# Kernel tuning notes

Measured on AMD Instinct MI355X. Metric: run time of the kernel, lower is better.

Reference implementation:

```python
import jax, jax.numpy as jnp
import numpy as np

B = 32768
ARITY = 6
E = 256          # embedding_size
NF = 512         # num_filters
NR = 50000       # num_roles
NV = 50000       # num_values
BN_EPS = 1e-5


def setup_inputs() -> dict:
    key = jax.random.key(0)
    ks = jax.random.split(key, 7)
    bound = (1.0 / E) ** 0.5
    # padding_idx=0 rows zeroed, matching torch Embedding(padding_idx=0)
    emb_roles = jax.random.uniform(ks[0], (NR, E), minval=-bound, maxval=bound).at[0].set(0.0)
    emb_values = jax.random.uniform(ks[1], (NV, E), minval=-bound, maxval=bound).at[2].set(0.0).at[0].set(0.0)
    # truncated_normal(std=0.1) approximated by clipped normal
    conv1_w = jnp.clip(jax.random.normal(ks[2], (NF, 2, E)), -2.0, 2.0) * 0.1
    conv2_w = jnp.clip(jax.random.normal(ks[3], (NF, 5, E)), -2.0, 2.0) * 0.1
    fc_w = jax.random.normal(ks[4], (1, NF)) * (2.0 / (NF + 1)) ** 0.5  # xavier_normal
    x_batch = jax.random.randint(ks[5], (B, 2 * ARITY), 0, NR, dtype=jnp.int32)
    return dict(
        x_batch=x_batch,
        arity=ARITY,
        emb_roles=emb_roles,
        emb_values=emb_values,
        conv1_w=conv1_w,
        conv1_b=jnp.zeros((NF,), jnp.float32),
        bn1_gamma=jnp.ones((NF,), jnp.float32),
        bn1_beta=jnp.zeros((NF,), jnp.float32),
        conv2_w=conv2_w,
        conv2_b=jnp.zeros((NF,), jnp.float32),
        bn2_gamma=jnp.ones((NF,), jnp.float32),
        bn2_beta=jnp.zeros((NF,), jnp.float32),
        fc_w=fc_w,
        fc_b=jnp.zeros((1,), jnp.float32),
    )


def _bn_relu(x, gamma, beta):
    # x: [B, K, F]; BatchNorm2d in training mode: per-(window-call, channel) stats over batch
    m = jnp.mean(x, axis=0, keepdims=True)
    v = jnp.var(x, axis=0, keepdims=True)  # biased, matches torch normalization
    return jax.nn.relu(gamma * (x - m) * jax.lax.rsqrt(v + BN_EPS) + beta)


def _forward(x_batch, arity, emb_roles, emb_values,
             conv1_w, conv1_b, bn1_gamma, bn1_beta,
             conv2_w, conv2_b, bn2_gamma, bn2_beta, fc_w, fc_b):
    roles = x_batch[:, 0::2]   # [B, arity]
    values = x_batch[:, 1::2]  # [B, arity]
    fr = emb_roles[roles[:, :2]]    # [B, 2, E]
    fv = emb_values[values[:, :2]]  # [B, 2, E]

    # conv1 on two (value, role) windows; kernel (2, E) collapses to a contraction over (2, E)
    win1 = jnp.stack([
        jnp.stack([fv[:, 0], fr[:, 0]], axis=1),
        jnp.stack([fv[:, 1], fr[:, 0]], axis=1),
    ], axis=1)  # [B, 2, 2, E]
    out1 = jnp.einsum('bkre,fre->bkf', win1, conv1_w) + conv1_b
    out1 = _bn_relu(out1, bn1_gamma, bn1_beta)  # [B, 2, F]

    if arity > 2:
        K = arity - 2
        kr = emb_roles[roles[:, 2:]]    # [B, K, E]
        kv = emb_values[values[:, 2:]]  # [B, K, E]
        hrt = jnp.stack([fv[:, 0], fr[:, 0], fv[:, 1]], axis=1)  # [B, 3, E]
        win2 = jnp.concatenate([
            jnp.broadcast_to(hrt[:, None], (hrt.shape[0], K, 3, hrt.shape[-1])),
            kr[:, :, None],
            kv[:, :, None],
        ], axis=2)  # [B, K, 5, E]
        out2 = jnp.einsum('bkre,fre->bkf', win2, conv2_w) + conv2_b
        out2 = _bn_relu(out2, bn2_gamma, bn2_beta)  # [B, K, F]
        allw = jnp.concatenate([out1, out2], axis=1)  # [B, 2+K, F]
    else:
        allw = out1

    min_val = jnp.min(allw, axis=1)  # [B, F]
    return min_val @ fc_w.T + fc_b   # [B, 1]


def reference(x_batch, arity, emb_roles, emb_values,
              conv1_w, conv1_b, bn1_gamma, bn1_beta,
              conv2_w, conv2_b, bn2_gamma, bn2_beta, fc_w, fc_b):
    return _forward(x_batch, arity, emb_roles, emb_values,
                    conv1_w, conv1_b, bn1_gamma, bn1_beta,
                    conv2_w, conv2_b, bn2_gamma, bn2_beta, fc_w, fc_b)
```

## Files before the change

### kernel.cpp

```cpp
#include <hip/hip_runtime.h>
#include <hip/hip_bf16.h>


typedef __hip_bfloat16 bf16;
typedef short bf16x8 __attribute__((ext_vector_type(8)));
typedef float f32x4 __attribute__((ext_vector_type(4)));

#define BATCH 32768

__device__ __forceinline__ unsigned short f2b(float f) {
    union { float f; unsigned u; } v; v.f = f;
    unsigned r = v.u + 0x7fffu + ((v.u >> 16) & 1u);
    return (unsigned short)(r >> 16);
}

__device__ __forceinline__ float b2f(unsigned short u) {
    union { unsigned x; float f; } v; v.x = ((unsigned)u) << 16;
    return v.f;
}

__global__ __launch_bounds__(256)
void cvt_kernel(const float* __restrict__ src, unsigned short* __restrict__ dst, int n4)
{
    int i = blockIdx.x * 256 + threadIdx.x;
    if (i >= n4) return;
    float4 v = ((const float4*)src)[i];
    ushort4 h;
    h.x = f2b(v.x); h.y = f2b(v.y); h.z = f2b(v.z); h.w = f2b(v.w);
    ((ushort4*)dst)[i] = h;
}

template<bool FINAL>
__global__ __launch_bounds__(512, 2)
void pass_kernel(const int* __restrict__ x, const bf16* __restrict__ embR,
                 const bf16* __restrict__ embV, const bf16* __restrict__ W1b,
                 const bf16* __restrict__ W2b, float* __restrict__ accum,
                 const float* __restrict__ coef, const float* __restrict__ fcw,
                 float* __restrict__ outacc)
{
    __shared__ __align__(16) short Ash[128 * 72];
    __shared__ __align__(16) short Bsh[256 * 72];
    __shared__ int xsh[384];
    __shared__ __align__(16) float scr[4096];

    const int tid = threadIdx.x;
    const int lin = blockIdx.x;
    const int mt  = (lin >> 4) * 8 + (lin & 7);
    const int nb  = ((lin >> 3) & 1) * 256;
    const int b0  = mt * 32;

    for (int i = tid; i < 384; i += 512) xsh[i] = x[b0 * 12 + i];
    if constexpr (!FINAL)
        for (int i = tid; i < 3072; i += 512) scr[i] = 0.f;
    __syncthreads();

    const int lane = tid & 63;
    const int wv   = tid >> 6;
    const int wmb  = (wv >> 2) * 64;
    const int wnb  = (wv & 3) * 64;
    const int quad = lane >> 4;
    const int l16  = lane & 15;

    auto stageA = [&](int seg, int col, bool g1) {
        #pragma unroll
        for (int it = 0; it < 2; ++it) {
            int flat = tid + it * 512;
            int row  = flat >> 3;
            int off8 = flat & 7;
            int idx; const bf16* tab;
            if (g1) {
                int vr = row & 63, bl = vr >> 1, kk = vr & 1;
                if (seg == 0) { idx = xsh[bl * 12 + 2 * kk + 1]; tab = embV; }
                else          { idx = xsh[bl * 12];              tab = embR; }
            } else {
                int bl = row >> 2, kk = row & 3;
                switch (seg) {
                    case 0:  idx = xsh[bl * 12 + 1];          tab = embV; break;
                    case 1:  idx = xsh[bl * 12 + 0];          tab = embR; break;
                    case 2:  idx = xsh[bl * 12 + 3];          tab = embV; break;
                    case 3:  idx = xsh[bl * 12 + 2 * kk + 4]; tab = embR; break;
                    default: idx = xsh[bl * 12 + 2 * kk + 5]; tab = embV; break;
                }
            }
            uint4 v = *((const uint4*)(tab + (size_t)idx * 256 + col) + off8);
            *(uint4*)&Ash[row * 72 + off8 * 8] = v;
        }
    };
    auto stageB = [&](const bf16* W, int stride, int col) {
        #pragma unroll
        for (int it = 0; it < 4; ++it) {
            int flat = tid + it * 512;
            int fr   = flat >> 3;
            int off8 = flat & 7;
            uint4 v = *((const uint4*)(W + (size_t)(nb + fr) * stride + col) + off8);
            *(uint4*)&Bsh[fr * 72 + off8 * 8] = v;
        }
    };
    auto mma = [&](f32x4 (&acc)[4][4]) {
        #pragma unroll
        for (int ks = 0; ks < 64; ks += 32) {
            bf16x8 af[4], bf_[4];
            #pragma unroll
            for (int t = 0; t < 4; ++t)
                af[t]  = *(const bf16x8*)&Ash[(wmb + t * 16 + l16) * 72 + ks + quad * 8];
            #pragma unroll
            for (int t = 0; t < 4; ++t)
                bf_[t] = *(const bf16x8*)&Bsh[(wnb + t * 16 + l16) * 72 + ks + quad * 8];
            #pragma unroll
            for (int i = 0; i < 4; ++i)
                #pragma unroll
                for (int j = 0; j < 4; ++j)
                    acc[i][j] = __builtin_amdgcn_mfma_f32_16x16x32_bf16(
                        af[i], bf_[j], acc[i][j], 0, 0, 0);
        }
    };

    f32x4 acc[4][4];

    #pragma unroll
    for (int i = 0; i < 4; ++i)
        #pragma unroll
        for (int j = 0; j < 4; ++j)
            acc[i][j] = (f32x4){0.f, 0.f, 0.f, 0.f};
    #pragma unroll 1
    for (int ch = 0; ch < 8; ++ch) {
        stageA(ch >> 2, (ch & 3) * 64, true);
        stageB(W1b, 512, ch * 64);
        __syncthreads();
        mma(acc);
        __syncthreads();
    }
    if (wv < 4) {
        if constexpr (!FINAL) {
            #pragma unroll
            for (int j = 0; j < 4; ++j) {
                int fl = wnb + j * 16 + l16;
                #pragma unroll
                for (int r = 0; r < 4; ++r) {
                    float sr = 0.f, qr = 0.f;
                    #pragma unroll
                    for (int i = 0; i < 4; ++i) {
                        float v = acc[i][j][r];
                        sr += v; qr += v * v;
                    }
                    atomicAdd(&scr[(r & 1) * 256 + fl], sr);
                    atomicAdd(&scr[1536 + (r & 1) * 256 + fl], qr);
                }
            }
        } else {
            unsigned short* m1s = (unsigned short*)scr;
            #pragma unroll
            for (int j = 0; j < 4; ++j) {
                int fl = wnb + j * 16 + l16, f = nb + fl;
                float a0 = coef[f],       c0 = coef[3072 + f];
                float a1 = coef[512 + f], c1 = coef[3584 + f];
                #pragma unroll
                for (int i = 0; i < 4; ++i)
                    #pragma unroll
                    for (int rp = 0; rp < 2; ++rp) {
                        int bl = i * 8 + quad * 2 + rp;
                        float v0 = fmaxf(a0 * acc[i][j][rp * 2]     + c0, 0.f);
                        float v1 = fmaxf(a1 * acc[i][j][rp * 2 + 1] + c1, 0.f);
                        m1s[bl * 256 + fl] = f2b(fminf(v0, v1));
                    }
            }
        }
    }

    #pragma unroll
    for (int i = 0; i < 4; ++i)
        #pragma unroll
        for (int j = 0; j < 4; ++j)
            acc[i][j] = (f32x4){0.f, 0.f, 0.f, 0.f};
    #pragma unroll 1
    for (int ch = 0; ch < 20; ++ch) {
        stageA(ch >> 2, (ch & 3) * 64, false);
        stageB(W2b, 1280, ch * 64);
        __syncthreads();
        mma(acc);
        __syncthreads();
    }
    if constexpr (!FINAL) {
        #pragma unroll
        for (int j = 0; j < 4; ++j) {
            int fl = wnb + j * 16 + l16;
            #pragma unroll
            for (int r = 0; r < 4; ++r) {
                float sr = 0.f, qr = 0.f;
                #pragma unroll
                for (int i = 0; i < 4; ++i) {
                    float v = acc[i][j][r];
                    sr += v; qr += v * v;
                }
                atomicAdd(&scr[(2 + r) * 256 + fl], sr);
                atomicAdd(&scr[1536 + (2 + r) * 256 + fl], qr);
            }
        }
        __syncthreads();
        for (int i2 = tid; i2 < 1536; i2 += 512) {
            int kw = i2 >> 8, fl = i2 & 255;
            atomicAdd(&accum[kw * 512 + nb + fl], scr[i2]);
            atomicAdd(&accum[3072 + kw * 512 + nb + fl], scr[1536 + i2]);
        }
    } else {
        const unsigned short* m1s = (const unsigned short*)scr;
        float dp[4] = {0.f, 0.f, 0.f, 0.f};
        #pragma unroll
        for (int j = 0; j < 4; ++j) {
            int fl = wnb + j * 16 + l16, f = nb + fl;
            float a[4], c[4];
            #pragma unroll
            for (int r = 0; r < 4; ++r) {
                a[r] = coef[(2 + r) * 512 + f];
                c[r] = coef[3072 + (2 + r) * 512 + f];
            }
            float fw = fcw[f];
            #pragma unroll
            for (int i = 0; i < 4; ++i) {
                int bb = (wmb >> 2) + i * 4 + quad;
                float mv = 1e30f;
                #pragma unroll
                for (int r = 0; r < 4; ++r)
                    mv = fminf(mv, fmaxf(a[r] * acc[i][j][r] + c[r], 0.f));
                mv = fminf(mv, b2f(m1s[bb * 256 + fl]));
                dp[i] += mv * fw;
            }
        }
        #pragma unroll
        for (int i = 0; i < 4; ++i) {
            float v = dp[i];
            v += __shfl_xor(v, 1); v += __shfl_xor(v, 2);
            v += __shfl_xor(v, 4); v += __shfl_xor(v, 8);
            if (l16 == 0)
                atomicAdd(&outacc[b0 + (wmb >> 2) + i * 4 + quad], v);
        }
    }
}

__global__ void bncoef_kernel(const float* __restrict__ accum,
                              const float* __restrict__ g1, const float* __restrict__ be1,
                              const float* __restrict__ g2, const float* __restrict__ be2,
                              float* __restrict__ coef)
{
    int id = blockIdx.x * 256 + threadIdx.x;
    if (id >= 3072) return;
    int kw = id >> 9, f = id & 511;
    float mean = accum[id] * (1.f / BATCH);
    float var  = accum[3072 + id] * (1.f / BATCH) - mean * mean;
    float g  = kw < 2 ? g1[f] : g2[f];
    float be = kw < 2 ? be1[f] : be2[f];
    float a  = g * rsqrtf(var + 1e-5f);
    coef[id] = a;
    coef[3072 + id] = be - a * mean;
}

__global__ void finish_kernel(const float* __restrict__ outacc,
                              const float* __restrict__ fcb, float* __restrict__ out)
{
    int b = blockIdx.x * 256 + threadIdx.x;
    if (b < BATCH)
        out[b] = outacc[b] + fcb[0];
}

extern "C" void kernel_launch(void* const* d_in, const int* in_sizes, int n_in,
                              void* d_out, int out_size, void* d_ws, size_t ws_size,
                              hipStream_t stream)
{
    (void)in_sizes; (void)n_in; (void)out_size; (void)ws_size;
    const int*   x    = (const int*)  d_in[0];
    const float* embR = (const float*)d_in[2];
    const float* embV = (const float*)d_in[3];
    const float* W1   = (const float*)d_in[4];
    const float* g1   = (const float*)d_in[6];
    const float* be1  = (const float*)d_in[7];
    const float* W2   = (const float*)d_in[8];
    const float* g2   = (const float*)d_in[10];
    const float* be2  = (const float*)d_in[11];
    const float* fcw  = (const float*)d_in[12];
    const float* fcb  = (const float*)d_in[13];

    char* wsb = (char*)d_ws;
    float* accum  = (float*)wsb;
    float* coef   = accum + 6144;
    float* outacc = coef + 6144;
    bf16*  Wbf1   = (bf16*)(wsb + 180224);
    bf16*  Wbf2   = (bf16*)(wsb + 704512);
    bf16*  embRb  = (bf16*)(wsb + 2015232);
    bf16*  embVb  = (bf16*)(wsb + 27615232);

    hipMemsetAsync(accum, 0, 6144 * sizeof(float), stream);
    hipMemsetAsync(outacc, 0, BATCH * sizeof(float), stream);
    cvt_kernel<<<256, 256, 0, stream>>>(W1, (unsigned short*)Wbf1, 65536);
    cvt_kernel<<<640, 256, 0, stream>>>(W2, (unsigned short*)Wbf2, 163840);
    cvt_kernel<<<12500, 256, 0, stream>>>(embR, (unsigned short*)embRb, 3200000);
    cvt_kernel<<<12500, 256, 0, stream>>>(embV, (unsigned short*)embVb, 3200000);

    pass_kernel<false><<<2048, 512, 0, stream>>>(
        x, embRb, embVb, Wbf1, Wbf2, accum, nullptr, nullptr, nullptr);
    bncoef_kernel<<<12, 256, 0, stream>>>(accum, g1, be1, g2, be2, coef);
    pass_kernel<true><<<2048, 512, 0, stream>>>(
        x, embRb, embVb, Wbf1, Wbf2, nullptr, coef, fcw, outacc);
    finish_kernel<<<128, 256, 0, stream>>>(outacc, fcb, (float*)d_out);
}
```

Before: 896.1 us.

## Fuse conv stages into one prefetched loop with full-filter 1024-thread blocks

Each block now covers all 512 filters with 16 waves instead of splitting filters across two blocks, so each embedding row is gathered once rather than twice. The conv1 and conv2 chunk loops merge into a single 28-stage loop. Global loads for the next stage are issued into registers before the current MFMA step, so gather latency overlaps with compute. The cost is more LDS per block (a doubled B tile and scratch), which likely allows only one block per CU, plus heavier barriers across 16 waves and extra register pressure from the prefetch buffers.

```diff
diff --git a/kernel.cpp b/kernel.cpp
--- a/kernel.cpp
+++ b/kernel.cpp
@@ -31,7 +31,7 @@
 }
 
 template<bool FINAL>
-__global__ __launch_bounds__(512, 2)
+__global__ __launch_bounds__(1024, 4)
 void pass_kernel(const int* __restrict__ x, const bf16* __restrict__ embR,
                  const bf16* __restrict__ embV, const bf16* __restrict__ W1b,
                  const bf16* __restrict__ W2b, float* __restrict__ accum,
@@ -39,64 +39,92 @@
                  float* __restrict__ outacc)
 {
     __shared__ __align__(16) short Ash[128 * 72];
-    __shared__ __align__(16) short Bsh[256 * 72];
+    __shared__ __align__(16) short Bsh[512 * 72];
     __shared__ int xsh[384];
-    __shared__ __align__(16) float scr[4096];
+    __shared__ __align__(16) float scr[8192];
 
     const int tid = threadIdx.x;
-    const int lin = blockIdx.x;
-    const int mt  = (lin >> 4) * 8 + (lin & 7);
-    const int nb  = ((lin >> 3) & 1) * 256;
-    const int b0  = mt * 32;
-
-    for (int i = tid; i < 384; i += 512) xsh[i] = x[b0 * 12 + i];
+    const int b0  = blockIdx.x * 32;
+
+    for (int i = tid; i < 384; i += 1024) xsh[i] = x[b0 * 12 + i];
     if constexpr (!FINAL)
-        for (int i = tid; i < 3072; i += 512) scr[i] = 0.f;
+        for (int i = tid; i < 6144; i += 1024) scr[i] = 0.f;
     __syncthreads();
 
     const int lane = tid & 63;
     const int wv   = tid >> 6;
-    const int wmb  = (wv >> 2) * 64;
-    const int wnb  = (wv & 3) * 64;
+    const int wmb  = (wv >> 3) * 64;
+    const int wnb  = (wv & 7) * 64;
     const int quad = lane >> 4;
     const int l16  = lane & 15;
-
-    auto stageA = [&](int seg, int col, bool g1) {
-        #pragma unroll
-        for (int it = 0; it < 2; ++it) {
-            int flat = tid + it * 512;
-            int row  = flat >> 3;
-            int off8 = flat & 7;
-            int idx; const bf16* tab;
-            if (g1) {
-                int vr = row & 63, bl = vr >> 1, kk = vr & 1;
-                if (seg == 0) { idx = xsh[bl * 12 + 2 * kk + 1]; tab = embV; }
-                else          { idx = xsh[bl * 12];              tab = embR; }
-            } else {
-                int bl = row >> 2, kk = row & 3;
-                switch (seg) {
-                    case 0:  idx = xsh[bl * 12 + 1];          tab = embV; break;
-                    case 1:  idx = xsh[bl * 12 + 0];          tab = embR; break;
-                    case 2:  idx = xsh[bl * 12 + 3];          tab = embV; break;
-                    case 3:  idx = xsh[bl * 12 + 2 * kk + 4]; tab = embR; break;
-                    default: idx = xsh[bl * 12 + 2 * kk + 5]; tab = embV; break;
-                }
-            }
-            uint4 v = *((const uint4*)(tab + (size_t)idx * 256 + col) + off8);
-            *(uint4*)&Ash[row * 72 + off8 * 8] = v;
+    const int arow = tid >> 3;
+    const int aoff = tid & 7;
+
+    auto issue = [&](int st, uint4& a, uint4 (&b)[4]) {
+        int idx; const bf16* tab;
+        if (st < 8) {
+            int seg = st >> 2;
+            int vr = arow & 63, bl = vr >> 1, kk = vr & 1;
+            if (seg == 0) { idx = xsh[bl * 12 + 2 * kk + 1]; tab = embV; }
+            else          { idx = xsh[bl * 12];              tab = embR; }
+            a = *((const uint4*)(tab + (size_t)idx * 256 + (st & 3) * 64) + aoff);
+            #pragma unroll
+            for (int it = 0; it < 4; ++it) {
+                int flat = tid + it * 1024, fr = flat >> 3, o8 = flat & 7;
+                b[it] = *((const uint4*)(W1b + (size_t)fr * 512 + st * 64) + o8);
+            }
+        } else if (st < 20) {
+            int ch = st - 8, seg = ch >> 2;
+            int bl = arow >> 2;
+            if (seg == 0)      { idx = xsh[bl * 12 + 1]; tab = embV; }
+            else if (seg == 1) { idx = xsh[bl * 12 + 0]; tab = embR; }
+            else               { idx = xsh[bl * 12 + 3]; tab = embV; }
+            a = *((const uint4*)(tab + (size_t)idx * 256 + (ch & 3) * 64) + aoff);
+            #pragma unroll
+            for (int it = 0; it < 4; ++it) {
+                int flat = tid + it * 1024, fr = flat >> 3, o8 = flat & 7;
+                b[it] = *((const uint4*)(W2b + (size_t)fr * 1280 + ch * 64) + o8);
+            }
+        } else {
+            int ch = st - 20, seg = ch >> 2;
+            int bl = arow >> 2, kk = arow & 3;
+            if (seg == 0) { idx = xsh[bl * 12 + 2 * kk + 4]; tab = embR; }
+            else          { idx = xsh[bl * 12 + 2 * kk + 5]; tab = embV; }
+            a = *((const uint4*)(tab + (size_t)idx * 256 + (ch & 3) * 64) + aoff);
+            #pragma unroll
+            for (int it = 0; it < 4; ++it) {
+                int flat = tid + it * 1024, fr = flat >> 3, o8 = flat & 7;
+                b[it] = *((const uint4*)(W2b + (size_t)fr * 1280 + 768 + ch * 64) + o8);
+            }
         }
     };
-    auto stageB = [&](const bf16* W, int stride, int col) {
+    auto wA = [&](const uint4& a) {
+        *(uint4*)&Ash[arow * 72 + aoff * 8] = a;
+    };
+    auto wB = [&](const uint4 (&b)[4]) {
         #pragma unroll
         for (int it = 0; it < 4; ++it) {
-            int flat = tid + it * 512;
-            int fr   = flat >> 3;
-            int off8 = flat & 7;
-            uint4 v = *((const uint4*)(W + (size_t)(nb + fr) * stride + col) + off8);
-            *(uint4*)&Bsh[fr * 72 + off8 * 8] = v;
+            int flat = tid + it * 1024, fr = flat >> 3, o8 = flat & 7;
+            *(uint4*)&Bsh[fr * 72 + o8 * 8] = b[it];
         }
     };
-    auto mma = [&](f32x4 (&acc)[4][4]) {
+
+    f32x4 acc[4][4];
+    #pragma unroll
+    for (int i = 0; i < 4; ++i)
+        #pragma unroll
+        for (int j = 0; j < 4; ++j)
+            acc[i][j] = (f32x4){0.f, 0.f, 0.f, 0.f};
+
+    uint4 pa, pb[4];
+    issue(0, pa, pb);
+
+    #pragma unroll 1
+    for (int st = 0; st < 28; ++st) {
+        wA(pa); wB(pb);
+        uint4 na, nb[4];
+        if (st < 27) issue(st + 1, na, nb);
+        __syncthreads();
         #pragma unroll
         for (int ks = 0; ks < 64; ks += 32) {
             bf16x8 af[4], bf_[4];
@@ -113,73 +141,57 @@
                     acc[i][j] = __builtin_amdgcn_mfma_f32_16x16x32_bf16(
                         af[i], bf_[j], acc[i][j], 0, 0, 0);
         }
-    };
-
-    f32x4 acc[4][4];
-
-    #pragma unroll
-    for (int i = 0; i < 4; ++i)
-        #pragma unroll
-        for (int j = 0; j < 4; ++j)
-            acc[i][j] = (f32x4){0.f, 0.f, 0.f, 0.f};
-    #pragma unroll 1
-    for (int ch = 0; ch < 8; ++ch) {
-        stageA(ch >> 2, (ch & 3) * 64, true);
-        stageB(W1b, 512, ch * 64);
+        if (st == 7) {
+            if (wv < 8) {
+                if constexpr (!FINAL) {
+                    #pragma unroll
+                    for (int j = 0; j < 4; ++j) {
+                        int fl = wnb + j * 16 + l16;
+                        #pragma unroll
+                        for (int r = 0; r < 4; ++r) {
+                            float sr = 0.f, qr = 0.f;
+                            #pragma unroll
+                            for (int i = 0; i < 4; ++i) {
+                                float v = acc[i][j][r];
+                                sr += v; qr += v * v;
+                            }
+                            atomicAdd(&scr[(r & 1) * 512 + fl], sr);
+                            atomicAdd(&scr[3072 + (r & 1) * 512 + fl], qr);
+                        }
+                    }
+                } else {
+                    unsigned short* m1s = (unsigned short*)scr;
+                    #pragma unroll
+                    for (int j = 0; j < 4; ++j) {
+                        int fl = wnb + j * 16 + l16;
+                        float a0 = coef[fl],       c0 = coef[3072 + fl];
+                        float a1 = coef[512 + fl], c1 = coef[3584 + fl];
+                        #pragma unroll
+                        for (int i = 0; i < 4; ++i)
+                            #pragma unroll
+                            for (int rp = 0; rp < 2; ++rp) {
+                                int bl = i * 8 + quad * 2 + rp;
+                                float v0 = fmaxf(a0 * acc[i][j][rp * 2]     + c0, 0.f);
+                                float v1 = fmaxf(a1 * acc[i][j][rp * 2 + 1] + c1, 0.f);
+                                m1s[bl * 512 + fl] = f2b(fminf(v0, v1));
+                            }
+                    }
+                }
+            }
+            #pragma unroll
+            for (int i = 0; i < 4; ++i)
+                #pragma unroll
+                for (int j = 0; j < 4; ++j)
+                    acc[i][j] = (f32x4){0.f, 0.f, 0.f, 0.f};
+        }
         __syncthreads();
-        mma(acc);
-        __syncthreads();
+        if (st < 27) {
+            pa = na;
+            #pragma unroll
+            for (int it = 0; it < 4; ++it) pb[it] = nb[it];
+        }
     }
-    if (wv < 4) {
-        if constexpr (!FINAL) {
-            #pragma unroll
-            for (int j = 0; j < 4; ++j) {
-                int fl = wnb + j * 16 + l16;
-                #pragma unroll
-                for (int r = 0; r < 4; ++r) {
-                    float sr = 0.f, qr = 0.f;
-                    #pragma unroll
-                    for (int i = 0; i < 4; ++i) {
-                        float v = acc[i][j][r];
-                        sr += v; qr += v * v;
-                    }
-                    atomicAdd(&scr[(r & 1) * 256 + fl], sr);
-                    atomicAdd(&scr[1536 + (r & 1) * 256 + fl], qr);
-                }
-            }
-        } else {
-            unsigned short* m1s = (unsigned short*)scr;
-            #pragma unroll
-            for (int j = 0; j < 4; ++j) {
-                int fl = wnb + j * 16 + l16, f = nb + fl;
-                float a0 = coef[f],       c0 = coef[3072 + f];
-                float a1 = coef[512 + f], c1 = coef[3584 + f];
-                #pragma unroll
-                for (int i = 0; i < 4; ++i)
-                    #pragma unroll
-                    for (int rp = 0; rp < 2; ++rp) {
-                        int bl = i * 8 + quad * 2 + rp;
-                        float v0 = fmaxf(a0 * acc[i][j][rp * 2]     + c0, 0.f);
-                        float v1 = fmaxf(a1 * acc[i][j][rp * 2 + 1] + c1, 0.f);
-                        m1s[bl * 256 + fl] = f2b(fminf(v0, v1));
-                    }
-            }
-        }
-    }
-
-    #pragma unroll
-    for (int i = 0; i < 4; ++i)
-        #pragma unroll
-        for (int j = 0; j < 4; ++j)
-            acc[i][j] = (f32x4){0.f, 0.f, 0.f, 0.f};
-    #pragma unroll 1
-    for (int ch = 0; ch < 20; ++ch) {
-        stageA(ch >> 2, (ch & 3) * 64, false);
-        stageB(W2b, 1280, ch * 64);
-        __syncthreads();
-        mma(acc);
-        __syncthreads();
-    }
+
     if constexpr (!FINAL) {
         #pragma unroll
         for (int j = 0; j < 4; ++j) {
@@ -192,22 +204,21 @@
                     float v = acc[i][j][r];
                     sr += v; qr += v * v;
                 }
-                atomicAdd(&scr[(2 + r) * 256 + fl], sr);
-                atomicAdd(&scr[1536 + (2 + r) * 256 + fl], qr);
+                atomicAdd(&scr[(2 + r) * 512 + fl], sr);
+                atomicAdd(&scr[3072 + (2 + r) * 512 + fl], qr);
             }
         }
         __syncthreads();
-        for (int i2 = tid; i2 < 1536; i2 += 512) {
-            int kw = i2 >> 8, fl = i2 & 255;
-            atomicAdd(&accum[kw * 512 + nb + fl], scr[i2]);
-            atomicAdd(&accum[3072 + kw * 512 + nb + fl], scr[1536 + i2]);
+        for (int i2 = tid; i2 < 3072; i2 += 1024) {
+            atomicAdd(&accum[i2], scr[i2]);
+            atomicAdd(&accum[3072 + i2], scr[3072 + i2]);
         }
     } else {
         const unsigned short* m1s = (const unsigned short*)scr;
         float dp[4] = {0.f, 0.f, 0.f, 0.f};
         #pragma unroll
         for (int j = 0; j < 4; ++j) {
-            int fl = wnb + j * 16 + l16, f = nb + fl;
+            int f = wnb + j * 16 + l16;
             float a[4], c[4];
             #pragma unroll
             for (int r = 0; r < 4; ++r) {
@@ -217,12 +228,12 @@
             float fw = fcw[f];
             #pragma unroll
             for (int i = 0; i < 4; ++i) {
-                int bb = (wmb >> 2) + i * 4 + quad;
+                int bb = 16 * (wv >> 3) + i * 4 + quad;
                 float mv = 1e30f;
                 #pragma unroll
                 for (int r = 0; r < 4; ++r)
                     mv = fminf(mv, fmaxf(a[r] * acc[i][j][r] + c[r], 0.f));
-                mv = fminf(mv, b2f(m1s[bb * 256 + fl]));
+                mv = fminf(mv, b2f(m1s[bb * 512 + f]));
                 dp[i] += mv * fw;
             }
         }
@@ -232,7 +243,7 @@
             v += __shfl_xor(v, 1); v += __shfl_xor(v, 2);
             v += __shfl_xor(v, 4); v += __shfl_xor(v, 8);
             if (l16 == 0)
-                atomicAdd(&outacc[b0 + (wmb >> 2) + i * 4 + quad], v);
+                atomicAdd(&outacc[b0 + 16 * (wv >> 3) + i * 4 + quad], v);
         }
     }
 }
@@ -295,10 +306,10 @@
     cvt_kernel<<<12500, 256, 0, stream>>>(embR, (unsigned short*)embRb, 3200000);
     cvt_kernel<<<12500, 256, 0, stream>>>(embV, (unsigned short*)embVb, 3200000);
 
-    pass_kernel<false><<<2048, 512, 0, stream>>>(
+    pass_kernel<false><<<1024, 1024, 0, stream>>>(
         x, embRb, embVb, Wbf1, Wbf2, accum, nullptr, nullptr, nullptr);
     bncoef_kernel<<<12, 256, 0, stream>>>(accum, g1, be1, g2, be2, coef);
-    pass_kernel<true><<<2048, 512, 0, stream>>>(
+    pass_kernel<true><<<1024, 1024, 0, stream>>>(
         x, embRb, embVb, Wbf1, Wbf2, nullptr, coef, fcw, outacc);
     finish_kernel<<<128, 256, 0, stream>>>(outacc, fcb, (float*)d_out);
 }
```

Measured after the change: 3.124 ms. +248.6%, slower.
